# Performance work log

Hardware: AMD Instinct MI355X
Metric: run time of the kernel (lower is better)

Reference implementation:

```python
import jax, jax.numpy as jnp
import numpy as np

EPS = 1e-5


def _conv_bn_relu(x, W, bn):
    # x: [B, Cin, N], W: [Cout, Cin] (1x1 conv), bn: [4, Cout] = (gamma, beta, mean, var)
    y = jnp.einsum('oi,bin->bon', W, x)
    g, b, m, v = bn[0], bn[1], bn[2], bn[3]
    y = g[:, None] * (y - m[:, None]) / jnp.sqrt(v[:, None] + EPS) + b[:, None]
    return jax.nn.relu(y)


def setup_inputs() -> dict:
    key = jax.random.key(0)
    ks = jax.random.split(key, 9)
    B, Cin, Cmid, Cout, N = 16, 131, 256, 128, 2048
    return {
        'features': jax.random.normal(ks[0], (B, Cin, N), dtype=jnp.float32),
        'Wq': jax.random.normal(ks[1], (Cmid, Cin), dtype=jnp.float32) * 0.05,
        'Wk': jax.random.normal(ks[2], (Cmid, Cin), dtype=jnp.float32) * 0.05,
        'Wv': jax.random.normal(ks[3], (Cmid, Cin), dtype=jnp.float32) * 0.05,
        'Wf': jax.random.normal(ks[4], (Cout, Cmid), dtype=jnp.float32) * 0.05,
        'bn_q': jax.random.uniform(ks[5], (4, Cmid), dtype=jnp.float32),
        'bn_k': jax.random.uniform(ks[6], (4, Cmid), dtype=jnp.float32),
        'bn_v': jax.random.uniform(ks[7], (4, Cmid), dtype=jnp.float32),
        'bn_f': jax.random.uniform(ks[8], (4, Cout), dtype=jnp.float32),
    }


def reference(features, Wq, Wk, Wv, Wf, bn_q, bn_k, bn_v, bn_f):
    q = _conv_bn_relu(features, Wq, bn_q)   # [B, 2C, N]
    k = _conv_bn_relu(features, Wk, bn_k)   # [B, 2C, N]
    v = _conv_bn_relu(features, Wv, bn_v)   # [B, 2C, N]
    # scores = Q^T K (no scaling, matching the original)
    scores = jnp.einsum('bcn,bcm->bnm', q, k)          # [B, N, N]
    weights = jax.nn.softmax(scores, axis=-1)
    attn = jnp.einsum('bnm,bcm->bcn', weights, v)      # [B, 2C, N]
    return _conv_bn_relu(attn, Wf, bn_f)               # [B, C, N]
```

## Files before the change

kernel.cpp:

```cpp
#include <hip/hip_runtime.h>

typedef __attribute__((ext_vector_type(4))) float f32x4;
typedef __attribute__((ext_vector_type(16))) float f32x16;
typedef __attribute__((ext_vector_type(8))) short short8;
typedef __attribute__((ext_vector_type(4))) unsigned short us4;
typedef unsigned short u16;
typedef unsigned int u32;
typedef _Float16 f16;
typedef __attribute__((ext_vector_type(8))) f16 f16x8;
typedef __attribute__((ext_vector_type(2))) __fp16 fp16x2;

#define B_   16
#define N_   2048
#define C_   256
#define CIN  131
#define COUT 128
#define L2E  1.44269504088896f

__device__ __forceinline__ u16 f2bf(float x) {
    u32 u = __float_as_uint(x);
    u32 r = (u + 0x7fffu + ((u >> 16) & 1u)) >> 16;
    return (u16)r;
}
__device__ __forceinline__ float bf2f(u16 h) {
    return __uint_as_float(((u32)h) << 16);
}
__device__ __forceinline__ u16 f2h(float x) {
    union { f16 h; u16 u; } c; c.h = (f16)x; return c.u;
}

__device__ __forceinline__ f32x4 mfma16(short8 a, short8 b, f32x4 c) {
    return __builtin_amdgcn_mfma_f32_16x16x32_bf16(a, b, c, 0, 0, 0);
}
__device__ __forceinline__ f32x4 mfma16h(f16x8 a, f16x8 b, f32x4 c) {
    return __builtin_amdgcn_mfma_f32_16x16x32_f16(a, b, c, 0, 0, 0);
}
__device__ __forceinline__ f32x16 mfma32(short8 a, short8 b, f32x16 c) {
    return __builtin_amdgcn_mfma_f32_32x32x16_bf16(a, b, c, 0, 0, 0);
}
__device__ __forceinline__ f32x16 mfma32h(f16x8 a, f16x8 b, f32x16 c) {
    return __builtin_amdgcn_mfma_f32_32x32x16_f16(a, b, c, 0, 0, 0);
}
__device__ __forceinline__ f32x16 z16() {
    f32x16 v;
    #pragma unroll
    for (int i = 0; i < 16; ++i) v[i] = 0.f;
    return v;
}
__device__ __forceinline__ u32 pkrtz(float a, float b) {
    fp16x2 r = __builtin_amdgcn_cvt_pkrtz(a, b);
    union { fp16x2 v; u32 u; } c; c.v = r; return c.u;
}

typedef __attribute__((address_space(1))) const unsigned int gu32;
typedef __attribute__((address_space(3))) unsigned int lu32;
__device__ __forceinline__ void gl_lds16(const u16* g, u16* l) {
    __builtin_amdgcn_global_load_lds((gu32*)g, (lu32*)l, 16, 0, 0);
}

#define RAW_BARRIER() do { asm volatile("" ::: "memory"); \
    __builtin_amdgcn_s_barrier(); \
    asm volatile("" ::: "memory"); } while (0)

__global__ __launch_bounds__(256) void w_prep(
    const float* __restrict__ Wq, const float* __restrict__ Wk,
    const float* __restrict__ Wv, const float* __restrict__ Wf,
    const float* __restrict__ bnq, const float* __restrict__ bnk,
    const float* __restrict__ bnv, const float* __restrict__ bnf,
    u16* __restrict__ wAh, u16* __restrict__ wAl,
    u16* __restrict__ wfh, u16* __restrict__ wfl,
    float* __restrict__ sqkv, float* __restrict__ tqkv,
    float* __restrict__ sf, float* __restrict__ tf)
{
    int t = threadIdx.x, l = t & 63;
    int g = blockIdx.x * 4 + (t >> 6);
    if (g < 240) {
        int m = g / 80, rem = g % 80, og = rem / 5, cc = rem % 5;
        const float* W = (m == 0) ? Wq : (m == 1) ? Wk : Wv;
        int o = og * 16 + (l & 15);
        size_t base = ((size_t)g * 64 + l) * 8;
        #pragma unroll
        for (int j = 0; j < 8; ++j) {
            int k = cc * 32 + (l >> 4) * 8 + j;
            float f = (k < CIN) ? W[o * CIN + k] : 0.f;
            u16 h = f2bf(f);
            wAh[base + j] = h;
            wAl[base + j] = f2bf(f - bf2f(h));
        }
    } else if (g < 304) {
        int u = g - 240;
        int o = (u >> 3) * 16 + (l & 15);
        int c0 = (u & 7) * 32 + (l >> 4) * 8;
        size_t base = ((size_t)u * 64 + l) * 8;
        #pragma unroll
        for (int j = 0; j < 8; ++j) {
            float f = Wf[o * 256 + c0 + j];
            u16 h = f2h(f);
            wfh[base + j] = h;
            union { f16 hh; u16 uu; } c; c.uu = h;
            wfl[base + j] = f2h(f - (float)c.hh);
        }
    }
    if (blockIdx.x == 0) {
        if (t < 256) {
            #pragma unroll
            for (int m = 0; m < 3; ++m) {
                const float* bn = (m == 0) ? bnq : (m == 1) ? bnk : bnv;
                float s = bn[t] * rsqrtf(bn[768 + t] + 1e-5f);
                sqkv[m * 256 + t] = s;
                tqkv[m * 256 + t] = bn[256 + t] - bn[512 + t] * s;
            }
        }
        if (t < 128) {
            float s = bnf[t] * rsqrtf(bnf[384 + t] + 1e-5f);
            sf[t] = s;
            tf[t] = bnf[128 + t] - bnf[256 + t] * s;
        }
    }
}

__global__ __launch_bounds__(256) void qkv_proj(
    const float* __restrict__ x,
    const u16* __restrict__ wAh, const u16* __restrict__ wAl,
    const float* __restrict__ sqkv, const float* __restrict__ tqkv,
    u16* __restrict__ qh, u16* __restrict__ ql,
    u16* __restrict__ kh, u16* __restrict__ kl, u16* __restrict__ vt)
{
    __shared__ __align__(16) float xs[64][164];

    int bid = blockIdx.x;
    int m  = bid >> 9;
    int r9 = bid & 511;
    int b = r9 >> 5, nt = r9 & 31;
    int t = threadIdx.x;
    int w = t >> 6, l = t & 63;
    int n0 = nt * 64;

    {
        int nb = (t & 15) * 4;
        for (int k = (t >> 4); k < CIN; k += 16) {
            f32x4 v = *(const f32x4*)(x + ((size_t)b * CIN + k) * N_ + n0 + nb);
            xs[nb + 0][k] = v[0]; xs[nb + 1][k] = v[1];
            xs[nb + 2][k] = v[2]; xs[nb + 3][k] = v[3];
        }
        for (int idx = t; idx < 64 * 29; idx += 256) {
            int n = idx / 29, k = CIN + idx % 29;
            xs[n][k] = 0.f;
        }
    }
    __syncthreads();

    f32x4 acc[4][4];
    #pragma unroll
    for (int og = 0; og < 4; ++og)
        #pragma unroll
        for (int njg = 0; njg < 4; ++njg) acc[og][njg] = (f32x4){0.f, 0.f, 0.f, 0.f};

    for (int cc = 0; cc < 5; ++cc) {
        short8 xbh[4], xbl[4];
        #pragma unroll
        for (int njg = 0; njg < 4; ++njg) {
            int n = njg * 16 + (l & 15);
            int k0 = cc * 32 + (l >> 4) * 8;
            f32x4 u0 = *(const f32x4*)&xs[n][k0];
            f32x4 u1 = *(const f32x4*)&xs[n][k0 + 4];
            u16 hh[8], ll[8];
            #pragma unroll
            for (int jj = 0; jj < 4; ++jj) {
                hh[jj] = f2bf(u0[jj]);     ll[jj] = f2bf(u0[jj] - bf2f(hh[jj]));
                hh[4 + jj] = f2bf(u1[jj]); ll[4 + jj] = f2bf(u1[jj] - bf2f(hh[4 + jj]));
            }
            short8 vh_, vl_;
            #pragma unroll
            for (int jj = 0; jj < 8; ++jj) { vh_[jj] = (short)hh[jj]; vl_[jj] = (short)ll[jj]; }
            xbh[njg] = vh_; xbl[njg] = vl_;
        }
        #pragma unroll
        for (int og = 0; og < 4; ++og) {
            size_t base = (((size_t)(m * 16 + w * 4 + og) * 5 + cc) * 64 + l) * 8;
            short8 ah  = *(const short8*)(wAh + base);
            short8 al4 = *(const short8*)(wAl + base);
            #pragma unroll
            for (int njg = 0; njg < 4; ++njg) {
                acc[og][njg] = mfma16(ah,  xbh[njg], acc[og][njg]);
                acc[og][njg] = mfma16(ah,  xbl[njg], acc[og][njg]);
                acc[og][njg] = mfma16(al4, xbh[njg], acc[og][njg]);
            }
        }
    }

    #pragma unroll
    for (int og = 0; og < 4; ++og) {
        int cb = (w * 4 + og) * 16 + (l >> 4) * 4;
        f32x4 sv = *(const f32x4*)(sqkv + m * 256 + cb);
        f32x4 tv = *(const f32x4*)(tqkv + m * 256 + cb);
        #pragma unroll
        for (int njg = 0; njg < 4; ++njg) {
            int n = n0 + njg * 16 + (l & 15);
            float z[4];
            #pragma unroll
            for (int r = 0; r < 4; ++r)
                z[r] = fmaxf(fmaf(acc[og][njg][r], sv[r], tv[r]), 0.f);
            if (m < 2) {
                size_t base = ((((size_t)b * 64 + (n >> 5)) * 16 + (cb >> 4)) * 64
                               + ((cb >> 3) & 1) * 32 + (n & 31)) * 8 + ((cb >> 2) & 1) * 4;
                u16 h0 = f2bf(z[0]), h1 = f2bf(z[1]), h2 = f2bf(z[2]), h3 = f2bf(z[3]);
                us4 hi4 = { h0, h1, h2, h3 };
                us4 lo4 = { f2bf(z[0] - bf2f(h0)), f2bf(z[1] - bf2f(h1)),
                            f2bf(z[2] - bf2f(h2)), f2bf(z[3] - bf2f(h3)) };
                *(us4*)((m ? kh : qh) + base) = hi4;
                *(us4*)((m ? kl : ql) + base) = lo4;
            } else {
                size_t base = ((((size_t)b * 128 + (n >> 4)) * 8 + (cb >> 5)) * 64
                               + ((cb >> 3) & 3) * 16 + (n & 15)) * 8 + (cb & 7);
                us4 v0 = { f2h(z[0]), f2h(z[1]), f2h(z[2]), f2h(z[3]) };
                *(us4*)(vt + base) = v0;
            }
        }
    }
}

__global__ __launch_bounds__(256) void vw_proj(
    const u16* __restrict__ vt,
    const u16* __restrict__ wfh, const u16* __restrict__ wfl,
    u16* __restrict__ vw)
{
    int bid = blockIdx.x;
    int b = bid >> 4, mt = bid & 15;
    int t = threadIdx.x, w = t >> 6, l = t & 63;

    f32x4 acc[2][8];
    #pragma unroll
    for (int oi = 0; oi < 2; ++oi)
        #pragma unroll
        for (int mg = 0; mg < 8; ++mg) acc[oi][mg] = (f32x4){0.f, 0.f, 0.f, 0.f};

    for (int cc = 0; cc < 8; ++cc) {
        f16x8 vtf[8];
        #pragma unroll
        for (int mg = 0; mg < 8; ++mg)
            vtf[mg] = *(const f16x8*)(vt + ((((size_t)b * 128 + mt * 8 + mg) * 8 + cc) * 64 + l) * 8);
        #pragma unroll
        for (int oi = 0; oi < 2; ++oi) {
            int og = w * 2 + oi;
            f16x8 bh = *(const f16x8*)(wfh + (((size_t)og * 8 + cc) * 64 + l) * 8);
            f16x8 bl = *(const f16x8*)(wfl + (((size_t)og * 8 + cc) * 64 + l) * 8);
            #pragma unroll
            for (int mg = 0; mg < 8; ++mg) {
                acc[oi][mg] = mfma16h(vtf[mg], bh, acc[oi][mg]);
                acc[oi][mg] = mfma16h(vtf[mg], bl, acc[oi][mg]);
            }
        }
    }

    #pragma unroll
    for (int oi = 0; oi < 2; ++oi) {
        int og = w * 2 + oi;
        int o = og * 16 + (l & 15);
        #pragma unroll
        for (int mg = 0; mg < 8; ++mg) {
            int mm0 = mt * 128 + mg * 16 + (l >> 4) * 4;
            size_t idx = ((((size_t)b * 64 + (mm0 >> 5)) * 4 + (o >> 5)) * 2 + ((mm0 >> 4) & 1)) * 512
                         + (size_t)(((mm0 >> 3) & 1) * 32 + (o & 31)) * 8 + (mm0 & 7);
            us4 v = { f2h(acc[oi][mg][0]), f2h(acc[oi][mg][1]),
                      f2h(acc[oi][mg][2]), f2h(acc[oi][mg][3]) };
            *(us4*)(vw + idx) = v;
        }
    }
}

__global__ __launch_bounds__(256, 1) void attn_fwd(
    const u16* __restrict__ qh, const u16* __restrict__ ql,
    const u16* __restrict__ kh, const u16* __restrict__ kl,
    const u16* __restrict__ vw,
    const float* __restrict__ sf, const float* __restrict__ tf,
    float* __restrict__ out)
{
    __shared__ __align__(16) u16 smem[41216];

    int bid = blockIdx.x;
    int swz = (bid & 7) * 32 + (bid >> 3);
    int b   = swz >> 4;
    int qt  = swz & 15;
    int tid = threadIdx.x;
    int w = tid >> 6, l = tid & 63;
    int h = l >> 5;
    int qw = qt * 4 + w;

    const u16* khb = kh + (size_t)b * 64 * 16 * 512;
    const u16* klb = kl + (size_t)b * 64 * 16 * 512;
    const u16* vwb = vw + (size_t)b * 64 * 8 * 512;

    auto stage = [&](int mc, int kbase, int vbase) {
        size_t ko = (size_t)mc * 16 * 512;
        #pragma unroll
        for (int i = 0; i < 8; ++i) {
            int g = w * 8 + i;
            const u16* src = ((g & 1) ? klb : khb) + ko + (size_t)(g >> 1) * 512 + l * 8;
            gl_lds16(src, &smem[kbase + g * 512]);
        }
        size_t vo = (size_t)mc * 8 * 512;
        #pragma unroll
        for (int i = 0; i < 2; ++i) {
            int f = w * 2 + i;
            gl_lds16(vwb + vo + (size_t)f * 512 + l * 8, &smem[vbase + f * 512]);
        }
    };

    short8 qfh[16], qfl[16];
    #pragma unroll
    for (int cc = 0; cc < 16; ++cc) {
        size_t o = (((size_t)b * 64 + qw) * 16 + cc) * 512 + (size_t)l * 8;
        qfh[cc] = *(const short8*)(qh + o);
        qfl[cc] = *(const short8*)(ql + o);
    }

    f32x16 O0 = z16(), O1 = z16(), O2 = z16(), O3 = z16();
    float mrow = -1e30f, lrow = 0.f;
    float* als = (float*)&smem[40960];
    int alb = w * 32;

    stage(0, 0, 32768);
    asm volatile("s_waitcnt vmcnt(0)" ::: "memory");
    __syncthreads();

    for (int mc = 0; mc < 64; ++mc) {
        int cur = mc & 1;
        int kbase = cur * 16384;
        int vbase = 32768 + cur * 4096;
        if (mc < 63) stage(mc + 1, (cur ^ 1) * 16384, 32768 + (cur ^ 1) * 4096);

        const short8* KF = (const short8*)&smem[kbase];
        f32x16 sE = z16(), sO = z16();
        #pragma unroll
        for (int cc = 0; cc < 16; cc += 2) {
            short8 ke_h = KF[(cc * 2 + 0) * 64 + l];
            short8 ke_l = KF[(cc * 2 + 1) * 64 + l];
            short8 ko_h = KF[(cc * 2 + 2) * 64 + l];
            short8 ko_l = KF[(cc * 2 + 3) * 64 + l];
            sE = mfma32(ke_h, qfh[cc], sE);
            sO = mfma32(ko_h, qfh[cc + 1], sO);
            sE = mfma32(ke_h, qfl[cc], sE);
            sO = mfma32(ko_h, qfl[cc + 1], sO);
            sE = mfma32(ke_l, qfh[cc], sE);
            sO = mfma32(ko_l, qfh[cc + 1], sO);
        }
        float s[16];
        #pragma unroll
        for (int r = 0; r < 16; ++r) s[r] = sE[r] + sO[r];

        float mx = s[0];
        #pragma unroll
        for (int r = 1; r < 16; ++r) mx = fmaxf(mx, s[r]);
        mx = fmaxf(mx, __shfl_xor(mx, 32));
        bool need = mx > mrow + 8.f;
        if (__any(need)) {
            float mn = fmaxf(mrow, mx);
            float al = exp2f((mrow - mn) * L2E);
            mrow = mn;
            lrow *= al;
            als[alb + (l & 31)] = al;
            asm volatile("s_waitcnt lgkmcnt(0)" ::: "memory");
            f32x4 aq[4];
            #pragma unroll
            for (int g = 0; g < 4; ++g)
                aq[g] = *(const f32x4*)&als[alb + 8 * g + 4 * h];
            #pragma unroll
            for (int r = 0; r < 16; ++r) {
                float f = aq[r >> 2][r & 3];
                O0[r] *= f; O1[r] *= f; O2[r] *= f; O3[r] *= f;
            }
        }
        float p[16], sum = 0.f;
        #pragma unroll
        for (int r = 0; r < 16; ++r) {
            p[r] = exp2f((s[r] - mrow) * L2E);
            sum += p[r];
        }
        sum += __shfl_xor(sum, 32);
        lrow += sum;

        f16x8 pa0, pa1;
        #pragma unroll
        for (int ks = 0; ks < 2; ++ks) {
            u32 L0 = pkrtz(p[8 * ks + 0], p[8 * ks + 1]);
            u32 L1 = pkrtz(p[8 * ks + 2], p[8 * ks + 3]);
            u32 H0 = pkrtz(p[8 * ks + 4], p[8 * ks + 5]);
            u32 H1 = pkrtz(p[8 * ks + 6], p[8 * ks + 7]);
            u32 pL0 = (u32)__shfl_xor((int)L0, 32);
            u32 pL1 = (u32)__shfl_xor((int)L1, 32);
            u32 pH0 = (u32)__shfl_xor((int)H0, 32);
            u32 pH1 = (u32)__shfl_xor((int)H1, 32);
            union { u32 w[4]; f16x8 v; } u;
            u.w[0] = h ? pH0 : L0;
            u.w[1] = h ? pH1 : L1;
            u.w[2] = h ? H0 : pL0;
            u.w[3] = h ? H1 : pL1;
            if (ks == 0) pa0 = u.v; else pa1 = u.v;
        }

        const f16x8* VWF = (const f16x8*)&smem[vbase];
        O0 = mfma32h(pa0, VWF[0 * 64 + l], O0);
        O1 = mfma32h(pa0, VWF[2 * 64 + l], O1);
        O2 = mfma32h(pa0, VWF[4 * 64 + l], O2);
        O3 = mfma32h(pa0, VWF[6 * 64 + l], O3);
        O0 = mfma32h(pa1, VWF[1 * 64 + l], O0);
        O1 = mfma32h(pa1, VWF[3 * 64 + l], O1);
        O2 = mfma32h(pa1, VWF[5 * 64 + l], O2);
        O3 = mfma32h(pa1, VWF[7 * 64 + l], O3);

        asm volatile("s_waitcnt vmcnt(0)" ::: "memory");
        RAW_BARRIER();
    }

    als[alb + (l & 31)] = 1.f / lrow;
    asm volatile("s_waitcnt lgkmcnt(0)" ::: "memory");
    f32x4 iv[4];
    #pragma unroll
    for (int g = 0; g < 4; ++g)
        iv[g] = *(const f32x4*)&als[alb + 8 * g + 4 * h];

    int n0 = qt * 128 + w * 32;
    #pragma unroll
    for (int ot = 0; ot < 4; ++ot) {
        const f32x16& Ov = (ot == 0) ? O0 : (ot == 1) ? O1 : (ot == 2) ? O2 : O3;
        int o = ot * 32 + (l & 31);
        float sc = sf[o], tb = tf[o];
        #pragma unroll
        for (int g = 0; g < 4; ++g) {
            f32x4 res;
            #pragma unroll
            for (int rr = 0; rr < 4; ++rr)
                res[rr] = fmaxf(fmaf(Ov[g * 4 + rr] * iv[g][rr], sc, tb), 0.f);
            *(f32x4*)(out + ((size_t)b * COUT + o) * N_ + n0 + 8 * g + 4 * h) = res;
        }
    }
}

extern "C" void kernel_launch(void* const* d_in, const int* in_sizes, int n_in,
                              void* d_out, int out_size, void* d_ws, size_t ws_size,
                              hipStream_t stream)
{
    const float* x   = (const float*)d_in[0];
    const float* Wq  = (const float*)d_in[1];
    const float* Wk  = (const float*)d_in[2];
    const float* Wv  = (const float*)d_in[3];
    const float* Wf  = (const float*)d_in[4];
    const float* bnq = (const float*)d_in[5];
    const float* bnk = (const float*)d_in[6];
    const float* bnv = (const float*)d_in[7];
    const float* bnf = (const float*)d_in[8];
    float* out = (float*)d_out;

    const size_t NBUF = (size_t)B_ * N_ * C_;
    u16* qh  = (u16*)d_ws;
    u16* ql  = qh + NBUF;
    u16* kh  = ql + NBUF;
    u16* kl  = kh + NBUF;
    u16* vt  = kl + NBUF;
    u16* vwb = vt + NBUF;
    u16* wfh = vwb + 4194304;
    u16* wfl = wfh + 32768;
    u16* wAh = wfl + 32768;
    u16* wAl = wAh + 122880;
    float* sqkv = (float*)(wAl + 122880);
    float* tqkv = sqkv + 768;
    float* sf   = tqkv + 768;
    float* tf   = sf + 128;

    w_prep<<<dim3(76), dim3(256), 0, stream>>>(Wq, Wk, Wv, Wf, bnq, bnk, bnv, bnf,
                                               wAh, wAl, wfh, wfl, sqkv, tqkv, sf, tf);
    qkv_proj<<<dim3(1536), dim3(256), 0, stream>>>(x, wAh, wAl, sqkv, tqkv,
                                                   qh, ql, kh, kl, vt);
    vw_proj<<<dim3(256), dim3(256), 0, stream>>>(vt, wfh, wfl, vwb);
    attn_fwd<<<dim3(256), dim3(256), 0, stream>>>(qh, ql, kh, kl, vwb,
                                                  sf, tf, out);
}
```

Before: 190.2 us.

## Split attention KV range across wave pairs and merge partial softmax states

Each block now handles 64 query rows with two wave pairs, each processing alternating key chunks (even/odd) with its own LDS buffer, and the partial softmax states are merged at the end through shared memory. The grid doubles to 512 blocks and launch bounds allow two blocks per CU, aimed at raising occupancy and overlapping K/VW staging with compute via finer-grained waits. The LDS alpha broadcast is replaced with ds_bpermute. The cost is an extra merge step, with more barrier coupling between the wave pairs and more register pressure at the two-blocks-per-CU target.

```diff
diff --git a/kernel.cpp b/kernel.cpp
--- a/kernel.cpp
+++ b/kernel.cpp
@@ -50,6 +50,9 @@
 __device__ __forceinline__ u32 pkrtz(float a, float b) {
     fp16x2 r = __builtin_amdgcn_cvt_pkrtz(a, b);
     union { fp16x2 v; u32 u; } c; c.v = r; return c.u;
+}
+__device__ __forceinline__ float bperm_f(int lane, float v) {
+    return __uint_as_float((u32)__builtin_amdgcn_ds_bpermute(lane * 4, (int)__float_as_uint(v)));
 }
 
 typedef __attribute__((address_space(1))) const unsigned int gu32;
@@ -269,40 +272,47 @@
     }
 }
 
-__global__ __launch_bounds__(256, 1) void attn_fwd(
+__global__ __launch_bounds__(256, 2) void attn_fwd(
     const u16* __restrict__ qh, const u16* __restrict__ ql,
     const u16* __restrict__ kh, const u16* __restrict__ kl,
     const u16* __restrict__ vw,
     const float* __restrict__ sf, const float* __restrict__ tf,
     float* __restrict__ out)
 {
-    __shared__ __align__(16) u16 smem[41216];
+    __shared__ __align__(16) u16 smem[40960];
 
     int bid = blockIdx.x;
-    int swz = (bid & 7) * 32 + (bid >> 3);
-    int b   = swz >> 4;
-    int qt  = swz & 15;
+    int swz = (bid & 7) * 64 + (bid >> 3);
+    int b   = swz >> 5;
+    int pt  = swz & 31;
     int tid = threadIdx.x;
     int w = tid >> 6, l = tid & 63;
     int h = l >> 5;
-    int qw = qt * 4 + w;
+    int p   = w >> 1;
+    int par = w & 1;
+    int qw  = pt * 2 + p;
 
     const u16* khb = kh + (size_t)b * 64 * 16 * 512;
     const u16* klb = kl + (size_t)b * 64 * 16 * 512;
     const u16* vwb = vw + (size_t)b * 64 * 8 * 512;
 
-    auto stage = [&](int mc, int kbase, int vbase) {
+    int kbase = par * 16384;
+    int vbase = 32768 + par * 4096;
+
+    auto stageK = [&](int mc) {
         size_t ko = (size_t)mc * 16 * 512;
         #pragma unroll
-        for (int i = 0; i < 8; ++i) {
-            int g = w * 8 + i;
+        for (int i = 0; i < 16; ++i) {
+            int g = p * 16 + i;
             const u16* src = ((g & 1) ? klb : khb) + ko + (size_t)(g >> 1) * 512 + l * 8;
             gl_lds16(src, &smem[kbase + g * 512]);
         }
+    };
+    auto stageVW = [&](int mc) {
         size_t vo = (size_t)mc * 8 * 512;
         #pragma unroll
-        for (int i = 0; i < 2; ++i) {
-            int f = w * 2 + i;
+        for (int i = 0; i < 4; ++i) {
+            int f = p * 4 + i;
             gl_lds16(vwb + vo + (size_t)f * 512 + l * 8, &smem[vbase + f * 512]);
         }
     };
@@ -317,18 +327,14 @@
 
     f32x16 O0 = z16(), O1 = z16(), O2 = z16(), O3 = z16();
     float mrow = -1e30f, lrow = 0.f;
-    float* als = (float*)&smem[40960];
-    int alb = w * 32;
-
-    stage(0, 0, 32768);
+
+    stageK(par);
+    stageVW(par);
     asm volatile("s_waitcnt vmcnt(0)" ::: "memory");
     __syncthreads();
 
-    for (int mc = 0; mc < 64; ++mc) {
-        int cur = mc & 1;
-        int kbase = cur * 16384;
-        int vbase = 32768 + cur * 4096;
-        if (mc < 63) stage(mc + 1, (cur ^ 1) * 16384, 32768 + (cur ^ 1) * 4096);
+    for (int r = 0; r < 32; ++r) {
+        int mc = 2 * r + par;
 
         const short8* KF = (const short8*)&smem[kbase];
         f32x16 sE = z16(), sO = z16();
@@ -347,11 +353,14 @@
         }
         float s[16];
         #pragma unroll
-        for (int r = 0; r < 16; ++r) s[r] = sE[r] + sO[r];
+        for (int r2 = 0; r2 < 16; ++r2) s[r2] = sE[r2] + sO[r2];
+
+        RAW_BARRIER();
+        if (r < 31) stageK(mc + 2);
 
         float mx = s[0];
         #pragma unroll
-        for (int r = 1; r < 16; ++r) mx = fmaxf(mx, s[r]);
+        for (int r2 = 1; r2 < 16; ++r2) mx = fmaxf(mx, s[r2]);
         mx = fmaxf(mx, __shfl_xor(mx, 32));
         bool need = mx > mrow + 8.f;
         if (__any(need)) {
@@ -359,23 +368,18 @@
             float al = exp2f((mrow - mn) * L2E);
             mrow = mn;
             lrow *= al;
-            als[alb + (l & 31)] = al;
-            asm volatile("s_waitcnt lgkmcnt(0)" ::: "memory");
-            f32x4 aq[4];
-            #pragma unroll
-            for (int g = 0; g < 4; ++g)
-                aq[g] = *(const f32x4*)&als[alb + 8 * g + 4 * h];
-            #pragma unroll
-            for (int r = 0; r < 16; ++r) {
-                float f = aq[r >> 2][r & 3];
-                O0[r] *= f; O1[r] *= f; O2[r] *= f; O3[r] *= f;
-            }
-        }
-        float p[16], sum = 0.f;
-        #pragma unroll
-        for (int r = 0; r < 16; ++r) {
-            p[r] = exp2f((s[r] - mrow) * L2E);
-            sum += p[r];
+            #pragma unroll
+            for (int j = 0; j < 16; ++j) {
+                int qp = 8 * (j >> 2) + 4 * h + (j & 3);
+                float f = bperm_f(qp, al);
+                O0[j] *= f; O1[j] *= f; O2[j] *= f; O3[j] *= f;
+            }
+        }
+        float pv[16], sum = 0.f;
+        #pragma unroll
+        for (int r2 = 0; r2 < 16; ++r2) {
+            pv[r2] = exp2f((s[r2] - mrow) * L2E);
+            sum += pv[r2];
         }
         sum += __shfl_xor(sum, 32);
         lrow += sum;
@@ -383,10 +387,10 @@
         f16x8 pa0, pa1;
         #pragma unroll
         for (int ks = 0; ks < 2; ++ks) {
-            u32 L0 = pkrtz(p[8 * ks + 0], p[8 * ks + 1]);
-            u32 L1 = pkrtz(p[8 * ks + 2], p[8 * ks + 3]);
-            u32 H0 = pkrtz(p[8 * ks + 4], p[8 * ks + 5]);
-            u32 H1 = pkrtz(p[8 * ks + 6], p[8 * ks + 7]);
+            u32 L0 = pkrtz(pv[8 * ks + 0], pv[8 * ks + 1]);
+            u32 L1 = pkrtz(pv[8 * ks + 2], pv[8 * ks + 3]);
+            u32 H0 = pkrtz(pv[8 * ks + 4], pv[8 * ks + 5]);
+            u32 H1 = pkrtz(pv[8 * ks + 6], pv[8 * ks + 7]);
             u32 pL0 = (u32)__shfl_xor((int)L0, 32);
             u32 pL1 = (u32)__shfl_xor((int)L1, 32);
             u32 pH0 = (u32)__shfl_xor((int)H0, 32);
@@ -399,6 +403,9 @@
             if (ks == 0) pa0 = u.v; else pa1 = u.v;
         }
 
+        if (r < 31) { asm volatile("s_waitcnt vmcnt(16)" ::: "memory"); }
+        else        { asm volatile("s_waitcnt vmcnt(0)"  ::: "memory"); }
+
         const f16x8* VWF = (const f16x8*)&smem[vbase];
         O0 = mfma32h(pa0, VWF[0 * 64 + l], O0);
         O1 = mfma32h(pa0, VWF[2 * 64 + l], O1);
@@ -411,28 +418,56 @@
 
         asm volatile("s_waitcnt vmcnt(0)" ::: "memory");
         RAW_BARRIER();
-    }
-
-    als[alb + (l & 31)] = 1.f / lrow;
-    asm volatile("s_waitcnt lgkmcnt(0)" ::: "memory");
-    f32x4 iv[4];
-    #pragma unroll
-    for (int g = 0; g < 4; ++g)
-        iv[g] = *(const f32x4*)&als[alb + 8 * g + 4 * h];
-
-    int n0 = qt * 128 + w * 32;
-    #pragma unroll
-    for (int ot = 0; ot < 4; ++ot) {
-        const f32x16& Ov = (ot == 0) ? O0 : (ot == 1) ? O1 : (ot == 2) ? O2 : O3;
-        int o = ot * 32 + (l & 31);
-        float sc = sf[o], tb = tf[o];
-        #pragma unroll
-        for (int g = 0; g < 4; ++g) {
-            f32x4 res;
-            #pragma unroll
-            for (int rr = 0; rr < 4; ++rr)
-                res[rr] = fmaxf(fmaf(Ov[g * 4 + rr] * iv[g][rr], sc, tb), 0.f);
-            *(f32x4*)(out + ((size_t)b * COUT + o) * N_ + n0 + 8 * g + 4 * h) = res;
+        if (r < 31) stageVW(mc + 2);
+    }
+
+    __syncthreads();
+    float* scr = (float*)smem;
+    if (par == 1) {
+        #pragma unroll
+        for (int ot = 0; ot < 4; ++ot) {
+            const f32x16& Ov = (ot == 0) ? O0 : (ot == 1) ? O1 : (ot == 2) ? O2 : O3;
+            #pragma unroll
+            for (int j = 0; j < 16; ++j)
+                scr[p * 4096 + (ot * 16 + j) * 64 + l] = Ov[j];
+        }
+        scr[8192 + p * 128 + l] = mrow;
+        scr[8192 + p * 128 + 64 + l] = lrow;
+    }
+    __syncthreads();
+    if (par == 0) {
+        float m_o = scr[8192 + p * 128 + l];
+        float l_o = scr[8192 + p * 128 + 64 + l];
+        float mm = fmaxf(mrow, m_o);
+        float ae = exp2f((mrow - mm) * L2E);
+        float ao = exp2f((m_o - mm) * L2E);
+        float inv = 1.f / (ae * lrow + ao * l_o);
+        float aev = ae * inv, aov = ao * inv;
+        float aer[16], aor[16];
+        #pragma unroll
+        for (int j = 0; j < 16; ++j) {
+            int qp = 8 * (j >> 2) + 4 * h + (j & 3);
+            aer[j] = bperm_f(qp, aev);
+            aor[j] = bperm_f(qp, aov);
+        }
+        int n0 = pt * 64 + p * 32;
+        #pragma unroll
+        for (int ot = 0; ot < 4; ++ot) {
+            const f32x16& Ov = (ot == 0) ? O0 : (ot == 1) ? O1 : (ot == 2) ? O2 : O3;
+            int o = ot * 32 + (l & 31);
+            float sc = sf[o], tb = tf[o];
+            #pragma unroll
+            for (int g = 0; g < 4; ++g) {
+                f32x4 res;
+                #pragma unroll
+                for (int rr = 0; rr < 4; ++rr) {
+                    int j = g * 4 + rr;
+                    float oo = scr[p * 4096 + (ot * 16 + j) * 64 + l];
+                    float mg = aer[j] * Ov[j] + aor[j] * oo;
+                    res[rr] = fmaxf(fmaf(mg, sc, tb), 0.f);
+                }
+                *(f32x4*)(out + ((size_t)b * COUT + o) * N_ + n0 + 8 * g + 4 * h) = res;
+            }
         }
     }
 }
@@ -473,6 +508,6 @@
     qkv_proj<<<dim3(1536), dim3(256), 0, stream>>>(x, wAh, wAl, sqkv, tqkv,
                                                    qh, ql, kh, kl, vt);
     vw_proj<<<dim3(256), dim3(256), 0, stream>>>(vt, wfh, wfl, vwb);
-    attn_fwd<<<dim3(256), dim3(256), 0, stream>>>(qh, ql, kh, kl, vwb,
+    attn_fwd<<<dim3(512), dim3(256), 0, stream>>>(qh, ql, kh, kl, vwb,
                                                   sf, tf, out);
 }
```

Result: slower. 276.7 us (+45.5%).
